# Kernel optimization log

Hardware: AMD Instinct MI355X
Metric: run time of the kernel (lower is better)

Reference implementation:

```python
import jax, jax.numpy as jnp
import numpy as np

B = 32
NODES = [200000, 1024, 256, 32]
CH = [1, 32, 64, 128]
EDGES = [2048000, 262144, 8192]
NCLS = 10


def _wn(V, g):
    # PyTorch weight_norm (dim=0): each output row rescaled to norm g[o]
    return g[:, None] * V / jnp.linalg.norm(V, axis=1, keepdims=True)


def _fgl(x, src, dst, n_out, W, b):
    # x: (B, C_in, N_in); sparse random-adjacency downsample then channel mix
    xt = jnp.moveaxis(x, 2, 0)                                   # (N_in, B, C_in)
    gathered = xt[src]                                           # (E, B, C_in)
    pooled = jax.ops.segment_sum(gathered, dst, num_segments=n_out)  # (N_out, B, C_in)
    return jnp.einsum('nbc,oc->bon', pooled, W) + b[None, :, None]   # (B, C_out, N_out)


def setup_inputs() -> dict:
    key = jax.random.key(0)
    ks = jax.random.split(key, 20)
    d = {}
    d['x'] = jax.random.normal(ks[0], (B, NODES[0]), jnp.float32)
    for i in range(3):
        e = EDGES[i]
        n_in, n_out = NODES[i], NODES[i + 1]
        d[f'edge_src{i}'] = jax.random.randint(ks[1 + 2 * i], (e,), 0, n_in, jnp.int32)
        d[f'edge_dst{i}'] = jnp.sort(jax.random.randint(ks[2 + 2 * i], (e,), 0, n_out, jnp.int32))
    for i in range(3):
        cin, cout = CH[i], CH[i + 1]
        d[f'V{i}'] = jax.random.normal(ks[7 + 3 * i], (cout, cin), jnp.float32) * 0.1
        d[f'g{i}'] = jnp.ones((cout,), jnp.float32)
        d[f'b{i}'] = jnp.zeros((cout,), jnp.float32)
    d['Vfc'] = jax.random.normal(ks[16], (NCLS, CH[-1] * NODES[-1]), jnp.float32) * 0.02
    d['gfc'] = jnp.ones((NCLS,), jnp.float32)
    d['bfc'] = jnp.zeros((NCLS,), jnp.float32)
    return d


def reference(x, edge_src0, edge_dst0, edge_src1, edge_dst1, edge_src2, edge_dst2,
              V0, g0, b0, V1, g1, b1, V2, g2, b2, Vfc, gfc, bfc):
    z = x[:, None, :]                                            # (B, 1, N_in)
    z = _fgl(z, edge_src0, edge_dst0, NODES[1], _wn(V0, g0), b0)  # (B, 32, 1024)
    z = _fgl(z, edge_src1, edge_dst1, NODES[2], _wn(V1, g1), b1)  # (B, 64, 256)
    z = _fgl(z, edge_src2, edge_dst2, NODES[3], _wn(V2, g2), b2)  # (B, 128, 32)
    flat = z.reshape(z.shape[0], -1)                             # (B, 4096)
    return flat @ _wn(Vfc, gfc).T + bfc                          # (B, NCLS)
```

## Files before the change

### kernel.cpp

```cpp
#include <hip/hip_runtime.h>
#include <math.h>

#define N0 200000
#define N1 1024
#define N2 256
#define N3 32
#define NE0 2048000
#define NE1 262144
#define NE2 8192
#define BATCH 32
#define NCLS 10
#define NB 4
#define SRC_PER_B 50000
#define TBLOCKS 3125

typedef _Float16 h2 __attribute__((ext_vector_type(2)));
typedef _Float16 h8 __attribute__((ext_vector_type(8)));

__device__ __forceinline__ int lower_bound_i(const int* __restrict__ a, int n, int key) {
    int lo = 0, hi = n;
    while (lo < hi) {
        int mid = (lo + hi) >> 1;
        if (a[mid] < key) lo = mid + 1; else hi = mid;
    }
    return lo;
}

__global__ __launch_bounds__(256) void k_pre(const float* __restrict__ x,
                                             h2* __restrict__ xt,
                                             const int* __restrict__ src,
                                             const int* __restrict__ dst,
                                             int* __restrict__ esrc,
                                             int* __restrict__ bstart) {
    const int tid = threadIdx.x;
    if (blockIdx.x < TBLOCKS) {
        __shared__ float tile[32][65];
        const int col0 = blockIdx.x * 64;
        const int c = tid & 63, r0 = tid >> 6;
        #pragma unroll
        for (int r = r0; r < 32; r += 4) {
            int col = col0 + c;
            tile[r][c] = (col < N0) ? x[r * N0 + col] : 0.f;
        }
        __syncthreads();
        const int bb = (tid & 15) * 2, c0 = tid >> 4;
        #pragma unroll
        for (int cc = c0; cc < 64; cc += 16) {
            int col = col0 + cc;
            if (col < N0) {
                h2 v;
                v[0] = (_Float16)tile[bb][cc];
                v[1] = (_Float16)tile[bb + 1][cc];
                xt[col * 16 + (bb >> 1)] = v;
            }
        }
        return;
    }
    const int n = blockIdx.x - TBLOCKS;
    const int e0 = lower_bound_i(dst, NE0, n);
    const int e1 = lower_bound_i(dst, NE0, n + 1);
    const int len = e1 - e0;
    const int wave = tid >> 6, lane = tid & 63;
    const int q0 = e0 + (len * wave) / 4;
    const int q1 = e0 + (len * (wave + 1)) / 4;
    __shared__ int wcnt[4][NB];
    __shared__ int wbase[4][NB];

    int c0 = 0, c1 = 0, c2 = 0, c3 = 0;
    for (int base = q0; base < q1; base += 64) {
        int e = base + lane;
        int b = -1;
        if (e < q1) b = src[e] / SRC_PER_B;
        c0 += __popcll(__ballot(b == 0));
        c1 += __popcll(__ballot(b == 1));
        c2 += __popcll(__ballot(b == 2));
        c3 += __popcll(__ballot(b == 3));
    }
    if (lane == 0) { wcnt[wave][0] = c0; wcnt[wave][1] = c1; wcnt[wave][2] = c2; wcnt[wave][3] = c3; }
    __syncthreads();
    if (tid == 0) {
        int acc = e0;
        #pragma unroll
        for (int b = 0; b < NB; ++b) {
            bstart[n * (NB + 1) + b] = acc;
            #pragma unroll
            for (int w = 0; w < 4; ++w) { wbase[w][b] = acc; acc += wcnt[w][b]; }
        }
        bstart[n * (NB + 1) + NB] = acc;
    }
    __syncthreads();

    int u0 = wbase[wave][0], u1 = wbase[wave][1], u2 = wbase[wave][2], u3 = wbase[wave][3];
    for (int base = q0; base < q1; base += 64) {
        int e = base + lane;
        int s = 0, b = -1;
        if (e < q1) { s = src[e]; b = s / SRC_PER_B; }
        unsigned long long m0 = __ballot(b == 0);
        unsigned long long m1 = __ballot(b == 1);
        unsigned long long m2 = __ballot(b == 2);
        unsigned long long m3 = __ballot(b == 3);
        unsigned long long lt = (1ull << lane) - 1ull;
        if (b == 0)      esrc[u0 + __popcll(m0 & lt)] = s;
        else if (b == 1) esrc[u1 + __popcll(m1 & lt)] = s;
        else if (b == 2) esrc[u2 + __popcll(m2 & lt)] = s;
        else if (b == 3) esrc[u3 + __popcll(m3 & lt)] = s;
        u0 += __popcll(m0); u1 += __popcll(m1); u2 += __popcll(m2); u3 += __popcll(m3);
    }
}

__global__ __launch_bounds__(128) void k_gather0s(const h8* __restrict__ table,
                                                  const int* __restrict__ esrc,
                                                  const int* __restrict__ bstart,
                                                  _Float16* __restrict__ p0p) {
    const int b = blockIdx.x & (NB - 1);
    const int n = blockIdx.x >> 2;
    const int q0 = bstart[n * (NB + 1) + b];
    const int q1 = bstart[n * (NB + 1) + b + 1];
    const int tid = threadIdx.x;
    const int b4 = tid & 3;
    const int g  = tid >> 2;
    float acc[8] = {0.f, 0.f, 0.f, 0.f, 0.f, 0.f, 0.f, 0.f};
    int e = q0 + g;
    for (; e + 96 < q1; e += 128) {
        int s0 = esrc[e];
        int s1 = esrc[e + 32];
        int s2 = esrc[e + 64];
        int s3 = esrc[e + 96];
        h8 v0 = table[s0 * 4 + b4];
        h8 v1 = table[s1 * 4 + b4];
        h8 v2 = table[s2 * 4 + b4];
        h8 v3 = table[s3 * 4 + b4];
        #pragma unroll
        for (int i = 0; i < 8; ++i)
            acc[i] += (float)v0[i] + (float)v1[i] + (float)v2[i] + (float)v3[i];
    }
    for (; e < q1; e += 32) {
        int s = esrc[e];
        h8 v = table[s * 4 + b4];
        #pragma unroll
        for (int i = 0; i < 8; ++i) acc[i] += (float)v[i];
    }
    __shared__ float red[32][33];
    #pragma unroll
    for (int i = 0; i < 8; ++i) red[g][b4 * 8 + i] = acc[i];
    __syncthreads();
    #pragma unroll
    for (int s = 16; s >= 1; s >>= 1) {
        if (g < s) {
            #pragma unroll
            for (int i = 0; i < 8; ++i)
                red[g][b4 * 8 + i] += red[g + s][b4 * 8 + i];
        }
        __syncthreads();
    }
    if (tid < 32) p0p[(b * N1 + n) * 32 + tid] = (_Float16)red[0][tid];
}

__global__ __launch_bounds__(256) void k_gather1(const h8* __restrict__ p0p,
                                                 const int* __restrict__ src,
                                                 const int* __restrict__ dst,
                                                 _Float16* __restrict__ out_h,
                                                 float* __restrict__ cnt_out) {
    const int n = blockIdx.x;
    const int e0 = lower_bound_i(dst, NE1, n);
    const int e1 = lower_bound_i(dst, NE1, n + 1);
    const int tid = threadIdx.x;
    const int b4 = tid & 3;
    const int g  = tid >> 2;
    float acc[8] = {0.f, 0.f, 0.f, 0.f, 0.f, 0.f, 0.f, 0.f};
    for (int e = e0 + g; e < e1; e += 64) {
        int s = src[e];
        h8 v0 = p0p[0 * N1 * 4 + s * 4 + b4];
        h8 v1 = p0p[1 * N1 * 4 + s * 4 + b4];
        h8 v2 = p0p[2 * N1 * 4 + s * 4 + b4];
        h8 v3 = p0p[3 * N1 * 4 + s * 4 + b4];
        #pragma unroll
        for (int i = 0; i < 8; ++i)
            acc[i] += ((float)v0[i] + (float)v1[i]) + ((float)v2[i] + (float)v3[i]);
    }
    __shared__ float red[64][33];
    #pragma unroll
    for (int i = 0; i < 8; ++i) red[g][b4 * 8 + i] = acc[i];
    __syncthreads();
    #pragma unroll
    for (int s = 32; s >= 1; s >>= 1) {
        if (g < s) {
            #pragma unroll
            for (int i = 0; i < 8; ++i)
                red[g][b4 * 8 + i] += red[g + s][b4 * 8 + i];
        }
        __syncthreads();
    }
    if (tid < 32) out_h[n * 32 + tid] = (_Float16)red[0][tid];
    else if (tid == 32) cnt_out[n] = (float)(e1 - e0);
}

__global__ __launch_bounds__(256) void k_gather2(const h8* __restrict__ table,
                                                 const int* __restrict__ src,
                                                 const int* __restrict__ dst,
                                                 const float* __restrict__ cnt_in,
                                                 float* __restrict__ out_f,
                                                 float* __restrict__ cnt_out,
                                                 float* __restrict__ t_out) {
    const int n = blockIdx.x;
    const int e0 = lower_bound_i(dst, NE2, n);
    const int e1 = lower_bound_i(dst, NE2, n + 1);
    const int tid = threadIdx.x;
    const int b4 = tid & 3;
    const int g  = tid >> 2;
    float acc[8] = {0.f, 0.f, 0.f, 0.f, 0.f, 0.f, 0.f, 0.f};
    float tacc = 0.f;
    for (int e = e0 + g; e < e1; e += 64) {
        int s = src[e];
        h8 v = table[s * 4 + b4];
        #pragma unroll
        for (int i = 0; i < 8; ++i) acc[i] += (float)v[i];
        if (b4 == 0) tacc += cnt_in[s];
    }
    __shared__ float red[64][33];
    __shared__ float tred[64];
    #pragma unroll
    for (int i = 0; i < 8; ++i) red[g][b4 * 8 + i] = acc[i];
    if (b4 == 0) tred[g] = tacc;
    __syncthreads();
    #pragma unroll
    for (int s = 32; s >= 1; s >>= 1) {
        if (g < s) {
            #pragma unroll
            for (int i = 0; i < 8; ++i)
                red[g][b4 * 8 + i] += red[g + s][b4 * 8 + i];
            if (b4 == 0) tred[g] += tred[g + s];
        }
        __syncthreads();
    }
    if (tid < 32) out_f[n * 32 + tid] = red[0][tid];
    else if (tid == 32) cnt_out[n] = (float)(e1 - e0);
    else if (tid == 33) t_out[n] = tred[0];
}

__global__ __launch_bounds__(256) void k_out(
    const float* __restrict__ V0, const float* __restrict__ g0, const float* __restrict__ b0,
    const float* __restrict__ V1, const float* __restrict__ g1, const float* __restrict__ b1,
    const float* __restrict__ V2, const float* __restrict__ g2, const float* __restrict__ b2,
    const float* __restrict__ Vfc, const float* __restrict__ gfc, const float* __restrict__ bfc,
    const float* __restrict__ S2, const float* __restrict__ T2, const float* __restrict__ cnt2,
    float* __restrict__ out) {
    const int k = blockIdx.x;
    const int tid = threadIdx.x;
    __shared__ float w0[32], u[64], v[64], p[128], q[128], r[128];
    __shared__ float redA[8][32], redB[8][32], redC[8][32], redD[8][32];
    __shared__ float nnred[4];
    __shared__ float M[32];
    __shared__ float scale_s, Kc_s;

    if (tid < 32) {
        float val = V0[tid];
        w0[tid] = g0[tid] * val / fabsf(val);
    }
    __syncthreads();
    if (tid < 64) {
        float nn = 0.f;
        #pragma unroll
        for (int c = 0; c < 32; ++c) { float t = V1[tid * 32 + c]; nn += t * t; }
        float inv = g1[tid] * rsqrtf(nn);
        float su = 0.f, sv = 0.f;
        #pragma unroll
        for (int c = 0; c < 32; ++c) {
            float w = V1[tid * 32 + c] * inv;
            su += w * w0[c]; sv += w * b0[c];
        }
        u[tid] = su; v[tid] = sv;
    }
    __syncthreads();
    if (tid < 128) {
        float nn = 0.f;
        #pragma unroll
        for (int c = 0; c < 64; ++c) { float t = V2[tid * 64 + c]; nn += t * t; }
        float inv = g2[tid] * rsqrtf(nn);
        float sp = 0.f, sq = 0.f, sr = 0.f;
        #pragma unroll
        for (int c = 0; c < 64; ++c) {
            float w = V2[tid * 64 + c] * inv;
            sp += w * u[c]; sq += w * v[c]; sr += w * b1[c];
        }
        p[tid] = sp; q[tid] = sq; r[tid] = sr;
    }
    __syncthreads();

    const int n3 = tid & 31, og = tid >> 5;
    float nn = 0.f, mk = 0.f, mq = 0.f, mr = 0.f, mb = 0.f;
    #pragma unroll
    for (int i = 0; i < 16; ++i) {
        int o = og + 8 * i;
        float w = Vfc[k * 4096 + tid + 256 * i];
        nn += w * w;
        mk += w * p[o]; mq += w * q[o]; mr += w * r[o]; mb += w * b2[o];
    }
    #pragma unroll
    for (int off = 32; off; off >>= 1) nn += __shfl_xor(nn, off);
    if ((tid & 63) == 0) nnred[tid >> 6] = nn;
    redA[og][n3] = mk; redB[og][n3] = mq; redC[og][n3] = mr; redD[og][n3] = mb;
    __syncthreads();
    if (tid == 0) {
        float s = nnred[0] + nnred[1] + nnred[2] + nnred[3];
        scale_s = gfc[k] * rsqrtf(s);
    }
    __syncthreads();
    if (tid < 32) {
        float smk = 0.f, smq = 0.f, smr = 0.f, smb = 0.f;
        #pragma unroll
        for (int i = 0; i < 8; ++i) {
            smk += redA[i][tid]; smq += redB[i][tid];
            smr += redC[i][tid]; smb += redD[i][tid];
        }
        float scale = scale_s;
        M[tid] = scale * smk;
        float kcp = scale * (smq * T2[tid] + smr * cnt2[tid] + smb);
        #pragma unroll
        for (int off = 16; off; off >>= 1) kcp += __shfl_xor(kcp, off);
        if (tid == 0) Kc_s = kcp + bfc[k];
    }
    __syncthreads();
    if (tid < 32) {
        int b = tid;
        float s = 0.f;
        #pragma unroll
        for (int n = 0; n < 32; ++n) s += M[n] * S2[n * 32 + b];
        out[b * NCLS + k] = s + Kc_s;
    }
}

extern "C" void kernel_launch(void* const* d_in, const int* in_sizes, int n_in,
                              void* d_out, int out_size, void* d_ws, size_t ws_size,
                              hipStream_t stream) {
    const float* x   = (const float*)d_in[0];
    const int* src0  = (const int*)d_in[1];
    const int* dst0  = (const int*)d_in[2];
    const int* src1  = (const int*)d_in[3];
    const int* dst1  = (const int*)d_in[4];
    const int* src2  = (const int*)d_in[5];
    const int* dst2  = (const int*)d_in[6];
    const float* V0  = (const float*)d_in[7];
    const float* g0  = (const float*)d_in[8];
    const float* b0  = (const float*)d_in[9];
    const float* V1  = (const float*)d_in[10];
    const float* g1  = (const float*)d_in[11];
    const float* b1  = (const float*)d_in[12];
    const float* V2  = (const float*)d_in[13];
    const float* g2  = (const float*)d_in[14];
    const float* b2  = (const float*)d_in[15];
    const float* Vfc = (const float*)d_in[16];
    const float* gfc = (const float*)d_in[17];
    const float* bfc = (const float*)d_in[18];

    char* ws = (char*)d_ws;
    _Float16* xt   = (_Float16*)(ws);
    int* esrc      = (int*)(ws + 12800000);
    int* bstart    = (int*)(ws + 20992000);
    _Float16* P0p  = (_Float16*)(ws + 21012480);
    _Float16* S1h  = (_Float16*)(ws + 21274624);
    float* cnt1    = (float*)(ws + 21291008);
    float* S2      = (float*)(ws + 21292032);
    float* T2      = (float*)(ws + 21296128);
    float* cnt2    = (float*)(ws + 21296256);

    k_pre<<<TBLOCKS + N1, 256, 0, stream>>>(x, (h2*)xt, src0, dst0, esrc, bstart);
    k_gather0s<<<N1 * NB, 128, 0, stream>>>((const h8*)xt, esrc, bstart,
                                            (_Float16*)P0p);
    k_gather1<<<N2, 256, 0, stream>>>((const h8*)P0p, src1, dst1, S1h, cnt1);
    k_gather2<<<N3, 256, 0, stream>>>((const h8*)S1h, src2, dst2, cnt1,
                                      S2, cnt2, T2);
    k_out<<<NCLS, 256, 0, stream>>>(V0, g0, b0, V1, g1, b1, V2, g2, b2,
                                    Vfc, gfc, bfc, S2, T2, cnt2, (float*)d_out);
}
```

Before: 79.11 us.

## Interleave partition and transpose blocks in k_pre; move weight folding into gather1

The k_pre block indices are reordered so that every fourth block among the first 4096 does edge partitioning and the rest do transpose tiles. This interleaves the two kinds of work across the grid instead of running the partition blocks last. The weight-norm folding chain (V0..Vfc) moves out of the final kernel into extra blocks of the gather1 launch, where it runs alongside the gather. The final kernel then only combines the precomputed M/Q/R/B terms with S2, which shortens the serial tail. The cost is extra workspace buffers and a larger gather1 launch.

```diff
diff --git a/kernel.cpp b/kernel.cpp
--- a/kernel.cpp
+++ b/kernel.cpp
@@ -13,6 +13,7 @@
 #define NB 4
 #define SRC_PER_B 50000
 #define TBLOCKS 3125
+#define PREBLOCKS 4149
 
 typedef _Float16 h2 __attribute__((ext_vector_type(2)));
 typedef _Float16 h8 __attribute__((ext_vector_type(8)));
@@ -32,10 +33,13 @@
                                              const int* __restrict__ dst,
                                              int* __restrict__ esrc,
                                              int* __restrict__ bstart) {
+    const int i = blockIdx.x;
     const int tid = threadIdx.x;
-    if (blockIdx.x < TBLOCKS) {
+    const bool isPart = ((i & 3) == 3) && (i < 4096);
+    if (!isPart) {
+        const int t = (i < 4096) ? (i - (i >> 2)) : (i - 1024);
         __shared__ float tile[32][65];
-        const int col0 = blockIdx.x * 64;
+        const int col0 = t * 64;
         const int c = tid & 63, r0 = tid >> 6;
         #pragma unroll
         for (int r = r0; r < 32; r += 4) {
@@ -56,7 +60,7 @@
         }
         return;
     }
-    const int n = blockIdx.x - TBLOCKS;
+    const int n = i >> 2;
     const int e0 = lower_bound_i(dst, NE0, n);
     const int e1 = lower_bound_i(dst, NE0, n + 1);
     const int len = e1 - e0;
@@ -156,43 +160,126 @@
     if (tid < 32) p0p[(b * N1 + n) * 32 + tid] = (_Float16)red[0][tid];
 }
 
-__global__ __launch_bounds__(256) void k_gather1(const h8* __restrict__ p0p,
-                                                 const int* __restrict__ src,
-                                                 const int* __restrict__ dst,
-                                                 _Float16* __restrict__ out_h,
-                                                 float* __restrict__ cnt_out) {
-    const int n = blockIdx.x;
-    const int e0 = lower_bound_i(dst, NE1, n);
-    const int e1 = lower_bound_i(dst, NE1, n + 1);
+__global__ __launch_bounds__(256) void k_gather1w(
+    const h8* __restrict__ p0p, const int* __restrict__ src,
+    const int* __restrict__ dst, _Float16* __restrict__ out_h,
+    float* __restrict__ cnt_out,
+    const float* __restrict__ V0, const float* __restrict__ g0, const float* __restrict__ b0,
+    const float* __restrict__ V1, const float* __restrict__ g1, const float* __restrict__ b1,
+    const float* __restrict__ V2, const float* __restrict__ g2, const float* __restrict__ b2,
+    const float* __restrict__ Vfc, const float* __restrict__ gfc,
+    float* __restrict__ M_, float* __restrict__ Q2_, float* __restrict__ R2_,
+    float* __restrict__ B4_) {
     const int tid = threadIdx.x;
-    const int b4 = tid & 3;
-    const int g  = tid >> 2;
-    float acc[8] = {0.f, 0.f, 0.f, 0.f, 0.f, 0.f, 0.f, 0.f};
-    for (int e = e0 + g; e < e1; e += 64) {
-        int s = src[e];
-        h8 v0 = p0p[0 * N1 * 4 + s * 4 + b4];
-        h8 v1 = p0p[1 * N1 * 4 + s * 4 + b4];
-        h8 v2 = p0p[2 * N1 * 4 + s * 4 + b4];
-        h8 v3 = p0p[3 * N1 * 4 + s * 4 + b4];
-        #pragma unroll
-        for (int i = 0; i < 8; ++i)
-            acc[i] += ((float)v0[i] + (float)v1[i]) + ((float)v2[i] + (float)v3[i]);
-    }
-    __shared__ float red[64][33];
-    #pragma unroll
-    for (int i = 0; i < 8; ++i) red[g][b4 * 8 + i] = acc[i];
-    __syncthreads();
-    #pragma unroll
-    for (int s = 32; s >= 1; s >>= 1) {
-        if (g < s) {
+    if (blockIdx.x < N2) {
+        const int n = blockIdx.x;
+        const int e0 = lower_bound_i(dst, NE1, n);
+        const int e1 = lower_bound_i(dst, NE1, n + 1);
+        const int b4 = tid & 3;
+        const int g  = tid >> 2;
+        float acc[8] = {0.f, 0.f, 0.f, 0.f, 0.f, 0.f, 0.f, 0.f};
+        for (int e = e0 + g; e < e1; e += 64) {
+            int s = src[e];
+            h8 v0 = p0p[0 * N1 * 4 + s * 4 + b4];
+            h8 v1 = p0p[1 * N1 * 4 + s * 4 + b4];
+            h8 v2 = p0p[2 * N1 * 4 + s * 4 + b4];
+            h8 v3 = p0p[3 * N1 * 4 + s * 4 + b4];
             #pragma unroll
             for (int i = 0; i < 8; ++i)
-                red[g][b4 * 8 + i] += red[g + s][b4 * 8 + i];
-        }
+                acc[i] += ((float)v0[i] + (float)v1[i]) + ((float)v2[i] + (float)v3[i]);
+        }
+        __shared__ float red[64][33];
+        #pragma unroll
+        for (int i = 0; i < 8; ++i) red[g][b4 * 8 + i] = acc[i];
         __syncthreads();
-    }
-    if (tid < 32) out_h[n * 32 + tid] = (_Float16)red[0][tid];
-    else if (tid == 32) cnt_out[n] = (float)(e1 - e0);
+        #pragma unroll
+        for (int s = 32; s >= 1; s >>= 1) {
+            if (g < s) {
+                #pragma unroll
+                for (int i = 0; i < 8; ++i)
+                    red[g][b4 * 8 + i] += red[g + s][b4 * 8 + i];
+            }
+            __syncthreads();
+        }
+        if (tid < 32) out_h[n * 32 + tid] = (_Float16)red[0][tid];
+        else if (tid == 32) cnt_out[n] = (float)(e1 - e0);
+        return;
+    }
+    const int k = blockIdx.x - N2;
+    __shared__ float w0[32], u[64], v[64], p[128], q[128], r[128];
+    __shared__ float redA[8][32], redB[8][32], redC[8][32], redD[8][32];
+    __shared__ float nnred[4];
+    __shared__ float scale_s;
+
+    if (tid < 32) {
+        float val = V0[tid];
+        w0[tid] = g0[tid] * val / fabsf(val);
+    }
+    __syncthreads();
+    if (tid < 64) {
+        float nn = 0.f;
+        #pragma unroll
+        for (int c = 0; c < 32; ++c) { float t = V1[tid * 32 + c]; nn += t * t; }
+        float inv = g1[tid] * rsqrtf(nn);
+        float su = 0.f, sv = 0.f;
+        #pragma unroll
+        for (int c = 0; c < 32; ++c) {
+            float w = V1[tid * 32 + c] * inv;
+            su += w * w0[c]; sv += w * b0[c];
+        }
+        u[tid] = su; v[tid] = sv;
+    }
+    __syncthreads();
+    if (tid < 128) {
+        float nn = 0.f;
+        #pragma unroll
+        for (int c = 0; c < 64; ++c) { float t = V2[tid * 64 + c]; nn += t * t; }
+        float inv = g2[tid] * rsqrtf(nn);
+        float sp = 0.f, sq = 0.f, sr = 0.f;
+        #pragma unroll
+        for (int c = 0; c < 64; ++c) {
+            float w = V2[tid * 64 + c] * inv;
+            sp += w * u[c]; sq += w * v[c]; sr += w * b1[c];
+        }
+        p[tid] = sp; q[tid] = sq; r[tid] = sr;
+    }
+    __syncthreads();
+
+    const int n3 = tid & 31, og = tid >> 5;
+    float nn = 0.f, mk = 0.f, mq = 0.f, mr = 0.f, mb = 0.f;
+    #pragma unroll
+    for (int i = 0; i < 16; ++i) {
+        int o = og + 8 * i;
+        float w = Vfc[k * 4096 + tid + 256 * i];
+        nn += w * w;
+        mk += w * p[o]; mq += w * q[o]; mr += w * r[o]; mb += w * b2[o];
+    }
+    #pragma unroll
+    for (int off = 32; off; off >>= 1) nn += __shfl_xor(nn, off);
+    if ((tid & 63) == 0) nnred[tid >> 6] = nn;
+    redA[og][n3] = mk; redB[og][n3] = mq; redC[og][n3] = mr; redD[og][n3] = mb;
+    __syncthreads();
+    if (tid == 0) {
+        float s = nnred[0] + nnred[1] + nnred[2] + nnred[3];
+        scale_s = gfc[k] * rsqrtf(s);
+    }
+    __syncthreads();
+    if (tid < 32) {
+        float smk = 0.f, smq = 0.f, smr = 0.f, smb = 0.f;
+        #pragma unroll
+        for (int i = 0; i < 8; ++i) {
+            smk += redA[i][tid]; smq += redB[i][tid];
+            smr += redC[i][tid]; smb += redD[i][tid];
+        }
+        float scale = scale_s;
+        M_[k * 32 + tid]  = scale * smk;
+        Q2_[k * 32 + tid] = scale * smq;
+        R2_[k * 32 + tid] = scale * smr;
+        float bs = scale * smb;
+        #pragma unroll
+        for (int off = 16; off; off >>= 1) bs += __shfl_xor(bs, off);
+        if (tid == 0) B4_[k] = bs;
+    }
 }
 
 __global__ __launch_bounds__(256) void k_gather2(const h8* __restrict__ table,
@@ -238,94 +325,30 @@
     else if (tid == 33) t_out[n] = tred[0];
 }
 
-__global__ __launch_bounds__(256) void k_out(
-    const float* __restrict__ V0, const float* __restrict__ g0, const float* __restrict__ b0,
-    const float* __restrict__ V1, const float* __restrict__ g1, const float* __restrict__ b1,
-    const float* __restrict__ V2, const float* __restrict__ g2, const float* __restrict__ b2,
-    const float* __restrict__ Vfc, const float* __restrict__ gfc, const float* __restrict__ bfc,
-    const float* __restrict__ S2, const float* __restrict__ T2, const float* __restrict__ cnt2,
-    float* __restrict__ out) {
+__global__ __launch_bounds__(64) void k_final(const float* __restrict__ M_,
+                                              const float* __restrict__ Q2_,
+                                              const float* __restrict__ R2_,
+                                              const float* __restrict__ B4_,
+                                              const float* __restrict__ bfc,
+                                              const float* __restrict__ S2,
+                                              const float* __restrict__ T2,
+                                              const float* __restrict__ cnt2,
+                                              float* __restrict__ out) {
     const int k = blockIdx.x;
     const int tid = threadIdx.x;
-    __shared__ float w0[32], u[64], v[64], p[128], q[128], r[128];
-    __shared__ float redA[8][32], redB[8][32], redC[8][32], redD[8][32];
-    __shared__ float nnred[4];
-    __shared__ float M[32];
-    __shared__ float scale_s, Kc_s;
-
-    if (tid < 32) {
-        float val = V0[tid];
-        w0[tid] = g0[tid] * val / fabsf(val);
-    }
-    __syncthreads();
-    if (tid < 64) {
-        float nn = 0.f;
-        #pragma unroll
-        for (int c = 0; c < 32; ++c) { float t = V1[tid * 32 + c]; nn += t * t; }
-        float inv = g1[tid] * rsqrtf(nn);
-        float su = 0.f, sv = 0.f;
-        #pragma unroll
-        for (int c = 0; c < 32; ++c) {
-            float w = V1[tid * 32 + c] * inv;
-            su += w * w0[c]; sv += w * b0[c];
-        }
-        u[tid] = su; v[tid] = sv;
-    }
-    __syncthreads();
-    if (tid < 128) {
-        float nn = 0.f;
-        #pragma unroll
-        for (int c = 0; c < 64; ++c) { float t = V2[tid * 64 + c]; nn += t * t; }
-        float inv = g2[tid] * rsqrtf(nn);
-        float sp = 0.f, sq = 0.f, sr = 0.f;
-        #pragma unroll
-        for (int c = 0; c < 64; ++c) {
-            float w = V2[tid * 64 + c] * inv;
-            sp += w * u[c]; sq += w * v[c]; sr += w * b1[c];
-        }
-        p[tid] = sp; q[tid] = sq; r[tid] = sr;
-    }
-    __syncthreads();
-
-    const int n3 = tid & 31, og = tid >> 5;
-    float nn = 0.f, mk = 0.f, mq = 0.f, mr = 0.f, mb = 0.f;
-    #pragma unroll
-    for (int i = 0; i < 16; ++i) {
-        int o = og + 8 * i;
-        float w = Vfc[k * 4096 + tid + 256 * i];
-        nn += w * w;
-        mk += w * p[o]; mq += w * q[o]; mr += w * r[o]; mb += w * b2[o];
-    }
-    #pragma unroll
-    for (int off = 32; off; off >>= 1) nn += __shfl_xor(nn, off);
-    if ((tid & 63) == 0) nnred[tid >> 6] = nn;
-    redA[og][n3] = mk; redB[og][n3] = mq; redC[og][n3] = mr; redD[og][n3] = mb;
-    __syncthreads();
-    if (tid == 0) {
-        float s = nnred[0] + nnred[1] + nnred[2] + nnred[3];
-        scale_s = gfc[k] * rsqrtf(s);
-    }
-    __syncthreads();
-    if (tid < 32) {
-        float smk = 0.f, smq = 0.f, smr = 0.f, smb = 0.f;
-        #pragma unroll
-        for (int i = 0; i < 8; ++i) {
-            smk += redA[i][tid]; smq += redB[i][tid];
-            smr += redC[i][tid]; smb += redD[i][tid];
-        }
-        float scale = scale_s;
-        M[tid] = scale * smk;
-        float kcp = scale * (smq * T2[tid] + smr * cnt2[tid] + smb);
-        #pragma unroll
-        for (int off = 16; off; off >>= 1) kcp += __shfl_xor(kcp, off);
-        if (tid == 0) Kc_s = kcp + bfc[k];
-    }
+    __shared__ float Kc_s;
+    float kc = 0.f;
+    if (tid < 32)
+        kc = Q2_[k * 32 + tid] * T2[tid] + R2_[k * 32 + tid] * cnt2[tid];
+    #pragma unroll
+    for (int off = 16; off; off >>= 1) kc += __shfl_xor(kc, off);
+    if (tid == 0) Kc_s = kc + B4_[k] + bfc[k];
     __syncthreads();
     if (tid < 32) {
         int b = tid;
         float s = 0.f;
         #pragma unroll
-        for (int n = 0; n < 32; ++n) s += M[n] * S2[n * 32 + b];
+        for (int n = 0; n < 32; ++n) s += M_[k * 32 + n] * S2[n * 32 + b];
         out[b * NCLS + k] = s + Kc_s;
     }
 }
@@ -363,13 +386,21 @@
     float* S2      = (float*)(ws + 21292032);
     float* T2      = (float*)(ws + 21296128);
     float* cnt2    = (float*)(ws + 21296256);
-
-    k_pre<<<TBLOCKS + N1, 256, 0, stream>>>(x, (h2*)xt, src0, dst0, esrc, bstart);
+    float* M_      = (float*)(ws + 21296384);
+    float* Q2_     = (float*)(ws + 21297664);
+    float* R2_     = (float*)(ws + 21298944);
+    float* B4_     = (float*)(ws + 21300224);
+
+    k_pre<<<PREBLOCKS, 256, 0, stream>>>(x, (h2*)xt, src0, dst0, esrc, bstart);
     k_gather0s<<<N1 * NB, 128, 0, stream>>>((const h8*)xt, esrc, bstart,
                                             (_Float16*)P0p);
-    k_gather1<<<N2, 256, 0, stream>>>((const h8*)P0p, src1, dst1, S1h, cnt1);
+    k_gather1w<<<N2 + NCLS, 256, 0, stream>>>((const h8*)P0p, src1, dst1,
+                                              S1h, cnt1,
+                                              V0, g0, b0, V1, g1, b1,
+                                              V2, g2, b2, Vfc, gfc,
+                                              M_, Q2_, R2_, B4_);
     k_gather2<<<N3, 256, 0, stream>>>((const h8*)S1h, src2, dst2, cnt1,
                                       S2, cnt2, T2);
-    k_out<<<NCLS, 256, 0, stream>>>(V0, g0, b0, V1, g1, b1, V2, g2, b2,
-                                    Vfc, gfc, bfc, S2, T2, cnt2, (float*)d_out);
-}
+    k_final<<<NCLS, 64, 0, stream>>>(M_, Q2_, R2_, B4_, bfc, S2, T2, cnt2,
+                                     (float*)d_out);
+}
```

Result: slower. 85.75 us (+8.4%).
